# Kernel tuning notes

Hardware: AMD Instinct MI355X
Metric: run time of the kernel (lower is better)

Reference implementation:

```python
import jax, jax.numpy as jnp
import numpy as np
import math


def setup_inputs() -> dict:
    key = jax.random.key(0)
    kq, kk, kv = jax.random.split(key, 3)
    shape = (4, 16, 2048, 64)  # [B, H, S, D]
    return {
        "q": jax.random.normal(kq, shape, dtype=jnp.float32),
        "k": jax.random.normal(kk, shape, dtype=jnp.float32),
        "v": jax.random.normal(kv, shape, dtype=jnp.float32),
    }


def reference(q, k, v):
    # Faithful to the torch module: exp(QK^T / sqrt(d)) then row-normalize
    # (no max-subtraction, matching the original math exactly).
    d = q.shape[-1]
    a = jnp.einsum('bhid,bhjd->bhij', q, k)          # [B,H,S,S]
    a = jnp.exp(a / jnp.float32(math.sqrt(float(d))))
    d_inv = 1.0 / jnp.sum(a, axis=-1, keepdims=True)  # [B,H,S,1]
    a_hat = d_inv * a
    return jnp.einsum('bhij,bhjd->bhid', a_hat, v)   # [B,H,S,D]
```

## Files before the change

kernel.cpp:

```cpp
#include <hip/hip_runtime.h>
#include <hip/hip_fp16.h>

typedef _Float16 half8  __attribute__((ext_vector_type(8)));
typedef _Float16 half4  __attribute__((ext_vector_type(4)));
typedef __fp16   fp16x2 __attribute__((ext_vector_type(2)));
typedef float    floatx4 __attribute__((ext_vector_type(4)));
typedef float    f32x16 __attribute__((ext_vector_type(16)));
typedef unsigned int uint4v __attribute__((ext_vector_type(4)));

#define SEQ    2048
#define HD     64
#define QTILE  256
#define KVB    64
#define PITCH  72
#define NXCD   8

__global__ __launch_bounds__(512, 4)
void attn_fwd(const float* __restrict__ Q, const float* __restrict__ K,
              const float* __restrict__ V, float* __restrict__ O) {
    const int nqt  = SEQ / QTILE;

    const int bid  = blockIdx.x;
    const int xcd  = bid & (NXCD - 1);
    const int slot = bid >> 3;
    const int work = xcd * ((int)gridDim.x >> 3) + slot;
    const int head = work / nqt;
    const int qti  = work % nqt;

    const size_t hoff = (size_t)head * SEQ * HD;
    const float* Qh = Q + hoff;
    const float* Kh = K + hoff;
    const float* Vh = V + hoff;
    float*       Oh = O + hoff;

    const int tid  = threadIdx.x;
    const int lane = tid & 63;
    const int w8   = tid >> 6;
    const int l31  = lane & 31;
    const int h    = lane >> 5;

    __shared__ __align__(16) _Float16 lds[2][2][KVB][PITCH];

    const int q0w = qti * QTILE + w8 * 32;

    const int kr  = tid >> 3;
    const int kc8 = (tid & 7) << 3;
    const int vd  = tid & 63;
    const int vr0 = (tid >> 6) << 3;

    const float QSCALE = 0.125f * 1.44269504f;
    half8 qf[4];
    {
        const float* qp = Qh + (size_t)(q0w + l31) * HD + h*8;
        #pragma unroll
        for (int ks = 0; ks < 4; ++ks) {
            floatx4 a = *(const floatx4*)(qp + ks*16);
            floatx4 b = *(const floatx4*)(qp + ks*16 + 4);
            fp16x2 h0 = __builtin_amdgcn_cvt_pkrtz(a[0]*QSCALE, a[1]*QSCALE);
            fp16x2 h1 = __builtin_amdgcn_cvt_pkrtz(a[2]*QSCALE, a[3]*QSCALE);
            fp16x2 h2 = __builtin_amdgcn_cvt_pkrtz(b[0]*QSCALE, b[1]*QSCALE);
            fp16x2 h3 = __builtin_amdgcn_cvt_pkrtz(b[2]*QSCALE, b[3]*QSCALE);
            half8 hh;
            hh[0]=h0[0]; hh[1]=h0[1]; hh[2]=h1[0]; hh[3]=h1[1];
            hh[4]=h2[0]; hh[5]=h2[1]; hh[6]=h3[0]; hh[7]=h3[1];
            qf[ks] = hh;
        }
    }

    f32x16 Oa0 = {}, Oa1 = {};
    float ps = 0.f;

    floatx4 kp0, kp1;
    float va0, va1, va2, va3, va4, va5, va6, va7;

#define ISSUE(KV)                                                            \
    do {                                                                     \
        const float* kbp = Kh + (size_t)(KV) * HD + (size_t)kr * HD + kc8;   \
        kp0 = *(const floatx4*)(kbp);                                        \
        kp1 = *(const floatx4*)(kbp + 4);                                    \
        const float* vbp = Vh + (size_t)(KV) * HD + (size_t)vr0 * HD + vd;   \
        va0 = vbp[0*HD]; va1 = vbp[1*HD]; va2 = vbp[2*HD]; va3 = vbp[3*HD];  \
        va4 = vbp[4*HD]; va5 = vbp[5*HD]; va6 = vbp[6*HD]; va7 = vbp[7*HD];  \
    } while (0)

#define STORE_ALL(BUF)                                                      \
    do {                                                                    \
        _Float16* Kb_ = &lds[BUF][0][0][0];                                 \
        _Float16* Vb_ = &lds[BUF][1][0][0];                                 \
        fp16x2 a0 = __builtin_amdgcn_cvt_pkrtz(kp0[0], kp0[1]);             \
        fp16x2 a1 = __builtin_amdgcn_cvt_pkrtz(kp0[2], kp0[3]);             \
        fp16x2 a2 = __builtin_amdgcn_cvt_pkrtz(kp1[0], kp1[1]);             \
        fp16x2 a3 = __builtin_amdgcn_cvt_pkrtz(kp1[2], kp1[3]);             \
        half8 kh8;                                                          \
        kh8[0]=a0[0]; kh8[1]=a0[1]; kh8[2]=a1[0]; kh8[3]=a1[1];             \
        kh8[4]=a2[0]; kh8[5]=a2[1]; kh8[6]=a3[0]; kh8[7]=a3[1];             \
        *(half8*)&Kb_[kr*PITCH + kc8] = kh8;                                \
        fp16x2 b0 = __builtin_amdgcn_cvt_pkrtz(va0, va1);                   \
        fp16x2 b1 = __builtin_amdgcn_cvt_pkrtz(va2, va3);                   \
        fp16x2 b2 = __builtin_amdgcn_cvt_pkrtz(va4, va5);                   \
        fp16x2 b3 = __builtin_amdgcn_cvt_pkrtz(va6, va7);                   \
        half8 vh8;                                                          \
        vh8[0]=b0[0]; vh8[1]=b0[1]; vh8[2]=b1[0]; vh8[3]=b1[1];             \
        vh8[4]=b2[0]; vh8[5]=b2[1]; vh8[6]=b3[0]; vh8[7]=b3[1];             \
        *(half8*)&Vb_[vd*PITCH + vr0] = vh8;                                \
    } while (0)

#define EXP2(X) __builtin_amdgcn_exp2f(X)

#define EXPPACK(S, PW, PSUM)                                                 \
    do {                                                                     \
        float e0_=EXP2((S)[ 0]), e1_=EXP2((S)[ 1]), e2_=EXP2((S)[ 2]), e3_=EXP2((S)[ 3]); \
        float e4_=EXP2((S)[ 4]), e5_=EXP2((S)[ 5]), e6_=EXP2((S)[ 6]), e7_=EXP2((S)[ 7]); \
        float e8_=EXP2((S)[ 8]), e9_=EXP2((S)[ 9]), ea_=EXP2((S)[10]), eb_=EXP2((S)[11]); \
        float ec_=EXP2((S)[12]), ed_=EXP2((S)[13]), ee_=EXP2((S)[14]), ef_=EXP2((S)[15]); \
        PSUM += ((e0_+e1_)+(e2_+e3_)) + ((e4_+e5_)+(e6_+e7_))                \
              + ((e8_+e9_)+(ea_+eb_)) + ((ec_+ed_)+(ee_+ef_));               \
        unsigned x0_ = __builtin_bit_cast(unsigned, __builtin_amdgcn_cvt_pkrtz(e0_, e1_)); \
        unsigned x1_ = __builtin_bit_cast(unsigned, __builtin_amdgcn_cvt_pkrtz(e2_, e3_)); \
        unsigned y0_ = __builtin_bit_cast(unsigned, __builtin_amdgcn_cvt_pkrtz(e4_, e5_)); \
        unsigned y1_ = __builtin_bit_cast(unsigned, __builtin_amdgcn_cvt_pkrtz(e6_, e7_)); \
        unsigned z0_ = __builtin_bit_cast(unsigned, __builtin_amdgcn_cvt_pkrtz(e8_, e9_)); \
        unsigned z1_ = __builtin_bit_cast(unsigned, __builtin_amdgcn_cvt_pkrtz(ea_, eb_)); \
        unsigned u0_ = __builtin_bit_cast(unsigned, __builtin_amdgcn_cvt_pkrtz(ec_, ed_)); \
        unsigned u1_ = __builtin_bit_cast(unsigned, __builtin_amdgcn_cvt_pkrtz(ee_, ef_)); \
        unsigned tx0_ = __shfl_xor(h ? x0_ : y0_, 32, 64);                   \
        unsigned tx1_ = __shfl_xor(h ? x1_ : y1_, 32, 64);                   \
        unsigned tz0_ = __shfl_xor(h ? z0_ : u0_, 32, 64);                   \
        unsigned tz1_ = __shfl_xor(h ? z1_ : u1_, 32, 64);                   \
        PW[0] = h ? tx0_ : x0_;  PW[1] = h ? tx1_ : x1_;                     \
        PW[2] = h ? y0_  : tx0_; PW[3] = h ? y1_  : tx1_;                    \
        PW[4] = h ? tz0_ : z0_;  PW[5] = h ? tz1_ : z1_;                     \
        PW[6] = h ? u0_  : tz0_; PW[7] = h ? u1_  : tz1_;                    \
    } while (0)

    ISSUE(0);
    STORE_ALL(0);

    for (int kv = 0; kv < SEQ; kv += KVB) {
        const int buf = (kv >> 6) & 1;

        __syncthreads();

        {
            const int kvn = (kv + KVB < SEQ) ? (kv + KVB) : kv;
            ISSUE(kvn);
        }

        const _Float16* Kb = &lds[buf][0][0][0];
        const _Float16* Vb = &lds[buf][1][0][0];

        #pragma unroll
        for (int kb = 0; kb < 2; ++kb) {
            f32x16 s = {};
            __builtin_amdgcn_s_setprio(1);
            #pragma unroll
            for (int ks = 0; ks < 4; ++ks) {
                half8 kf = *(const half8*)&Kb[(kb*32 + l31)*PITCH + ks*16 + h*8];
                s = __builtin_amdgcn_mfma_f32_32x32x16_f16(kf, qf[ks], s, 0, 0, 0);
            }
            __builtin_amdgcn_s_setprio(0);

            unsigned pw[8];
            EXPPACK(s, pw, ps);

            __builtin_amdgcn_s_setprio(1);
            #pragma unroll
            for (int kh2 = 0; kh2 < 2; ++kh2) {
                const int ks = kb*2 + kh2;
                half8 vb0 = *(const half8*)&Vb[( 0 + l31)*PITCH + ks*16 + h*8];
                half8 vb1 = *(const half8*)&Vb[(32 + l31)*PITCH + ks*16 + h*8];
                uint4v aw = { pw[kh2*4+0], pw[kh2*4+1], pw[kh2*4+2], pw[kh2*4+3] };
                half8 pa = __builtin_bit_cast(half8, aw);
                Oa0 = __builtin_amdgcn_mfma_f32_32x32x16_f16(pa, vb0, Oa0, 0, 0, 0);
                Oa1 = __builtin_amdgcn_mfma_f32_32x32x16_f16(pa, vb1, Oa1, 0, 0, 0);
            }
            __builtin_amdgcn_s_setprio(0);
        }

        STORE_ALL(buf ^ 1);
    }
#undef ISSUE
#undef STORE_ALL
#undef EXPPACK
#undef EXP2

    ps += __shfl_xor(ps, 32, 64);

    #pragma unroll
    for (int r = 0; r < 16; ++r) {
        const int co = (r & 3) + 8*(r >> 2);
        float inv = 1.0f / __shfl(ps, co + 4*h, 64);
        const size_t row = (size_t)(q0w + co + 4*h) * HD;
        Oh[row +  0 + l31] = Oa0[r] * inv;
        Oh[row + 32 + l31] = Oa1[r] * inv;
    }
}

extern "C" void kernel_launch(void* const* d_in, const int* in_sizes, int n_in,
                              void* d_out, int out_size, void* d_ws, size_t ws_size,
                              hipStream_t stream) {
    const float* q = (const float*)d_in[0];
    const float* k = (const float*)d_in[1];
    const float* v = (const float*)d_in[2];
    float* o = (float*)d_out;
    int nheads  = in_sizes[0] / (SEQ * HD);
    int nblocks = nheads * (SEQ / QTILE);
    attn_fwd<<<nblocks, 512, 0, stream>>>(q, k, v, o);
}
```

Baseline: 94.75 us.

## Halve query tile, drop LDS double buffering for single-buffer sync loop

Reduces the query tile from 256 to 128 rows with 256-thread blocks, doubling the grid and raising the occupancy target. It replaces the register-prefetched, double-buffered K/V LDS pipeline with a single buffer that is loaded, converted and stored each iteration between two barriers. This halves LDS per block and lowers register pressure so more blocks fit per CU. In exchange, global loads are no longer overlapped with the MFMA work inside a block, and each K/V tile is read by twice as many blocks.

```diff
diff --git a/kernel.cpp b/kernel.cpp
--- a/kernel.cpp
+++ b/kernel.cpp
@@ -2,7 +2,6 @@
 #include <hip/hip_fp16.h>
 
 typedef _Float16 half8  __attribute__((ext_vector_type(8)));
-typedef _Float16 half4  __attribute__((ext_vector_type(4)));
 typedef __fp16   fp16x2 __attribute__((ext_vector_type(2)));
 typedef float    floatx4 __attribute__((ext_vector_type(4)));
 typedef float    f32x16 __attribute__((ext_vector_type(16)));
@@ -10,12 +9,12 @@
 
 #define SEQ    2048
 #define HD     64
-#define QTILE  256
+#define QTILE  128
 #define KVB    64
 #define PITCH  72
 #define NXCD   8
 
-__global__ __launch_bounds__(512, 4)
+__global__ __launch_bounds__(256, 6)
 void attn_fwd(const float* __restrict__ Q, const float* __restrict__ K,
               const float* __restrict__ V, float* __restrict__ O) {
     const int nqt  = SEQ / QTILE;
@@ -35,18 +34,19 @@
 
     const int tid  = threadIdx.x;
     const int lane = tid & 63;
-    const int w8   = tid >> 6;
+    const int w    = tid >> 6;
     const int l31  = lane & 31;
     const int h    = lane >> 5;
 
-    __shared__ __align__(16) _Float16 lds[2][2][KVB][PITCH];
+    __shared__ __align__(16) _Float16 Klds[KVB][PITCH];
+    __shared__ __align__(16) _Float16 Vlds[HD][PITCH];
 
-    const int q0w = qti * QTILE + w8 * 32;
+    const int q0w = qti * QTILE + w * 32;
 
-    const int kr  = tid >> 3;
-    const int kc8 = (tid & 7) << 3;
-    const int vd  = tid & 63;
-    const int vr0 = (tid >> 6) << 3;
+    const int kr   = tid >> 2;
+    const int kc16 = (tid & 3) << 4;
+    const int vd   = tid & 63;
+    const int vr0  = (tid >> 6) << 4;
 
     const float QSCALE = 0.125f * 1.44269504f;
     half8 qf[4];
@@ -70,39 +70,14 @@
     f32x16 Oa0 = {}, Oa1 = {};
     float ps = 0.f;
 
-    floatx4 kp0, kp1;
-    float va0, va1, va2, va3, va4, va5, va6, va7;
-
-#define ISSUE(KV)                                                            \
-    do {                                                                     \
-        const float* kbp = Kh + (size_t)(KV) * HD + (size_t)kr * HD + kc8;   \
-        kp0 = *(const floatx4*)(kbp);                                        \
-        kp1 = *(const floatx4*)(kbp + 4);                                    \
-        const float* vbp = Vh + (size_t)(KV) * HD + (size_t)vr0 * HD + vd;   \
-        va0 = vbp[0*HD]; va1 = vbp[1*HD]; va2 = vbp[2*HD]; va3 = vbp[3*HD];  \
-        va4 = vbp[4*HD]; va5 = vbp[5*HD]; va6 = vbp[6*HD]; va7 = vbp[7*HD];  \
-    } while (0)
-
-#define STORE_ALL(BUF)                                                      \
+#define PACK8(D, X0, X1)                                                    \
     do {                                                                    \
-        _Float16* Kb_ = &lds[BUF][0][0][0];                                 \
-        _Float16* Vb_ = &lds[BUF][1][0][0];                                 \
-        fp16x2 a0 = __builtin_amdgcn_cvt_pkrtz(kp0[0], kp0[1]);             \
-        fp16x2 a1 = __builtin_amdgcn_cvt_pkrtz(kp0[2], kp0[3]);             \
-        fp16x2 a2 = __builtin_amdgcn_cvt_pkrtz(kp1[0], kp1[1]);             \
-        fp16x2 a3 = __builtin_amdgcn_cvt_pkrtz(kp1[2], kp1[3]);             \
-        half8 kh8;                                                          \
-        kh8[0]=a0[0]; kh8[1]=a0[1]; kh8[2]=a1[0]; kh8[3]=a1[1];             \
-        kh8[4]=a2[0]; kh8[5]=a2[1]; kh8[6]=a3[0]; kh8[7]=a3[1];             \
-        *(half8*)&Kb_[kr*PITCH + kc8] = kh8;                                \
-        fp16x2 b0 = __builtin_amdgcn_cvt_pkrtz(va0, va1);                   \
-        fp16x2 b1 = __builtin_amdgcn_cvt_pkrtz(va2, va3);                   \
-        fp16x2 b2 = __builtin_amdgcn_cvt_pkrtz(va4, va5);                   \
-        fp16x2 b3 = __builtin_amdgcn_cvt_pkrtz(va6, va7);                   \
-        half8 vh8;                                                          \
-        vh8[0]=b0[0]; vh8[1]=b0[1]; vh8[2]=b1[0]; vh8[3]=b1[1];             \
-        vh8[4]=b2[0]; vh8[5]=b2[1]; vh8[6]=b3[0]; vh8[7]=b3[1];             \
-        *(half8*)&Vb_[vd*PITCH + vr0] = vh8;                                \
+        fp16x2 p0_ = __builtin_amdgcn_cvt_pkrtz((X0)[0], (X0)[1]);          \
+        fp16x2 p1_ = __builtin_amdgcn_cvt_pkrtz((X0)[2], (X0)[3]);          \
+        fp16x2 p2_ = __builtin_amdgcn_cvt_pkrtz((X1)[0], (X1)[1]);          \
+        fp16x2 p3_ = __builtin_amdgcn_cvt_pkrtz((X1)[2], (X1)[3]);          \
+        D[0]=p0_[0]; D[1]=p0_[1]; D[2]=p1_[0]; D[3]=p1_[1];                 \
+        D[4]=p2_[0]; D[5]=p2_[1]; D[6]=p3_[0]; D[7]=p3_[1];                 \
     } while (0)
 
 #define EXP2(X) __builtin_amdgcn_exp2f(X)
@@ -133,21 +108,32 @@
         PW[6] = h ? u0_  : tz0_; PW[7] = h ? u1_  : tz1_;                    \
     } while (0)
 
-    ISSUE(0);
-    STORE_ALL(0);
-
     for (int kv = 0; kv < SEQ; kv += KVB) {
-        const int buf = (kv >> 6) & 1;
-
         __syncthreads();
 
         {
-            const int kvn = (kv + KVB < SEQ) ? (kv + KVB) : kv;
-            ISSUE(kvn);
+            const float* kbp = Kh + (size_t)(kv + kr) * HD + kc16;
+            floatx4 k0 = *(const floatx4*)(kbp);
+            floatx4 k1 = *(const floatx4*)(kbp + 4);
+            floatx4 k2 = *(const floatx4*)(kbp + 8);
+            floatx4 k3 = *(const floatx4*)(kbp + 12);
+            const float* vbp = Vh + (size_t)(kv + vr0) * HD + vd;
+            floatx4 v0 = { vbp[0*HD], vbp[1*HD], vbp[2*HD], vbp[3*HD] };
+            floatx4 v1 = { vbp[4*HD], vbp[5*HD], vbp[6*HD], vbp[7*HD] };
+            floatx4 v2 = { vbp[8*HD], vbp[9*HD], vbp[10*HD], vbp[11*HD] };
+            floatx4 v3 = { vbp[12*HD], vbp[13*HD], vbp[14*HD], vbp[15*HD] };
+            half8 kh0, kh1, vh0, vh1;
+            PACK8(kh0, k0, k1);
+            PACK8(kh1, k2, k3);
+            *(half8*)&Klds[kr][kc16]     = kh0;
+            *(half8*)&Klds[kr][kc16 + 8] = kh1;
+            PACK8(vh0, v0, v1);
+            PACK8(vh1, v2, v3);
+            *(half8*)&Vlds[vd][vr0]     = vh0;
+            *(half8*)&Vlds[vd][vr0 + 8] = vh1;
         }
 
-        const _Float16* Kb = &lds[buf][0][0][0];
-        const _Float16* Vb = &lds[buf][1][0][0];
+        __syncthreads();
 
         #pragma unroll
         for (int kb = 0; kb < 2; ++kb) {
@@ -155,7 +141,7 @@
             __builtin_amdgcn_s_setprio(1);
             #pragma unroll
             for (int ks = 0; ks < 4; ++ks) {
-                half8 kf = *(const half8*)&Kb[(kb*32 + l31)*PITCH + ks*16 + h*8];
+                half8 kf = *(const half8*)&Klds[kb*32 + l31][ks*16 + h*8];
                 s = __builtin_amdgcn_mfma_f32_32x32x16_f16(kf, qf[ks], s, 0, 0, 0);
             }
             __builtin_amdgcn_s_setprio(0);
@@ -167,20 +153,17 @@
             #pragma unroll
             for (int kh2 = 0; kh2 < 2; ++kh2) {
                 const int ks = kb*2 + kh2;
-                half8 vb0 = *(const half8*)&Vb[( 0 + l31)*PITCH + ks*16 + h*8];
-                half8 vb1 = *(const half8*)&Vb[(32 + l31)*PITCH + ks*16 + h*8];
+                half8 vf0 = *(const half8*)&Vlds[ 0 + l31][ks*16 + h*8];
+                half8 vf1 = *(const half8*)&Vlds[32 + l31][ks*16 + h*8];
                 uint4v aw = { pw[kh2*4+0], pw[kh2*4+1], pw[kh2*4+2], pw[kh2*4+3] };
                 half8 pa = __builtin_bit_cast(half8, aw);
-                Oa0 = __builtin_amdgcn_mfma_f32_32x32x16_f16(pa, vb0, Oa0, 0, 0, 0);
-                Oa1 = __builtin_amdgcn_mfma_f32_32x32x16_f16(pa, vb1, Oa1, 0, 0, 0);
+                Oa0 = __builtin_amdgcn_mfma_f32_32x32x16_f16(pa, vf0, Oa0, 0, 0, 0);
+                Oa1 = __builtin_amdgcn_mfma_f32_32x32x16_f16(pa, vf1, Oa1, 0, 0, 0);
             }
             __builtin_amdgcn_s_setprio(0);
         }
-
-        STORE_ALL(buf ^ 1);
     }
-#undef ISSUE
-#undef STORE_ALL
+#undef PACK8
 #undef EXPPACK
 #undef EXP2
 
@@ -205,5 +188,5 @@
     float* o = (float*)d_out;
     int nheads  = in_sizes[0] / (SEQ * HD);
     int nblocks = nheads * (SEQ / QTILE);
-    attn_fwd<<<nblocks, 512, 0, stream>>>(q, k, v, o);
+    attn_fwd<<<nblocks, 256, 0, stream>>>(q, k, v, o);
 }
```

Result: slower. 156.3 us (+64.9%).
